# Optimization experiments

Hardware: AMD Instinct MI355X
Metric: run time of the kernel (lower is better)

## Reference

```python
import jax, jax.numpy as jnp
import numpy as np

B, C, L = 16, 128, 512
F = L // 2 + 1  # 257

def setup_inputs() -> dict:
    key = jax.random.key(0)
    k1, k2, k3 = jax.random.split(key, 3)
    x = jax.random.normal(k1, (B, C, L), dtype=jnp.float32)
    A = jax.random.normal(k2, (F, F), dtype=jnp.float32)
    gumbel_u = jax.random.uniform(k3, (B, C, C, 2), dtype=jnp.float32)
    return {"x": x, "A": A, "gumbel_u": gumbel_u}

def reference(x, A, gumbel_u):
    # --- calculate_prob_distance ---
    xf = jnp.abs(jnp.fft.rfft(x, axis=-1))                 # (b, c, f)
    diff = xf[:, None, :, :] - xf[:, :, None, :]           # (b, c, c, f): x1 - x2
    temp = jnp.einsum('bijf,gf->bijg', diff, A)            # diff @ A.T
    dist = jnp.sum(temp * temp, axis=-1)                   # (b, c, c)
    exp_dist = 1.0 / (dist + 3e-8)
    c = exp_dist.shape[-1]
    eye = jnp.eye(c, dtype=exp_dist.dtype)
    exp_dist = exp_dist * (1.0 - eye)
    exp_max = jax.lax.stop_gradient(jnp.max(exp_dist, axis=-1, keepdims=True))
    p = exp_dist / (exp_max + 1e-8)
    p = (p + eye) * 0.99
    # --- bernoulli_gumbel_rsample (hard gumbel-softmax, tau=1) ---
    logits = jnp.log(p + 1e-8) - jnp.log(1.0 - p + 1e-8)
    logits_pair = jnp.stack([logits, -logits], axis=-1)    # (b, c, c, 2)
    g = -jnp.log(-jnp.log(gumbel_u + 1e-20) + 1e-20)       # gumbel noise
    y = jax.nn.softmax(logits_pair + g, axis=-1)
    y_hard = jax.nn.one_hot(jnp.argmax(y, axis=-1), 2, dtype=y.dtype)
    samples = y_hard + y - jax.lax.stop_gradient(y)        # straight-through
    binary_mask = samples[..., 0]                          # (b, c, c)
    mask = binary_mask[:, None, :, :]                      # (b, 1, c, c)
    return mask
```

## Files before the change

### kernel.cpp

```cpp
#include <hip/hip_runtime.h>

#define LN   512
#define FB   257
#define CB   128
#define NROW 2048
#define KF   260
#define NP   272
#define GC   8

typedef double double4_t __attribute__((ext_vector_type(4)));

__global__ __launch_bounds__(256)
void k_prep(const float* __restrict__ A, double* __restrict__ At_d,
            double* __restrict__ xft, double2* __restrict__ tw) {
    const int bx = blockIdx.x;
    if (bx < 277) {
        int idx = bx * 256 + threadIdx.x;
        if (idx < KF * NP) {
            int f = idx / NP, g = idx - f * NP;
            At_d[idx] = (f < FB && g < FB) ? (double)A[g * FB + f] : 0.0;
        }
    } else if (bx < 301) {
        int idx = (bx - 277) * 256 + threadIdx.x;
        xft[(size_t)FB * NROW + idx] = 0.0;
    } else {
        int j = threadIdx.x;
        const double PI = 3.14159265358979323846264338327950288;
        double s, c;
        sincos(-2.0 * PI * (double)j / 512.0, &s, &c);
        tw[j] = make_double2(c, s);
    }
}

__global__ __launch_bounds__(128)
void k_fft2(const float* __restrict__ x,
            const double2* __restrict__ twg,
            double* __restrict__ xft) {
    __shared__ double2 a[LN];
    __shared__ double2 tw[256];
    const int pair = blockIdx.x;
    const int tid  = threadIdx.x;
    const int r0   = pair * 2;

    for (int t = tid; t < 256; t += 128) tw[t] = twg[t];

    const float* x0 = x + (size_t)r0 * LN;
    const float* x1 = x0 + LN;
    #pragma unroll
    for (int q = 0; q < 4; ++q) {
        int n = tid + 128 * q;
        int r = (int)(__brev((unsigned)n) >> 23);
        a[r] = make_double2((double)x0[n], (double)x1[n]);
    }
    __syncthreads();

    for (int s = 1; s <= 9; ++s) {
        const int half   = 1 << (s - 1);
        const int tshift = 9 - s;
        #pragma unroll
        for (int u = 0; u < 2; ++u) {
            int t   = tid + 128 * u;
            int k   = t & (half - 1);
            int grp = t >> (s - 1);
            int p0  = (grp << s) + k;
            int p1  = p0 + half;
            double2 w  = tw[k << tshift];
            double2 uu = a[p0];
            double2 v  = a[p1];
            double vr = v.x * w.x - v.y * w.y;
            double vi = v.x * w.y + v.y * w.x;
            a[p0] = make_double2(uu.x + vr, uu.y + vi);
            a[p1] = make_double2(uu.x - vr, uu.y - vi);
        }
        __syncthreads();
    }

    for (int k = tid; k < FB; k += 128) {
        int m = (LN - k) & (LN - 1);
        double2 zk = a[k];
        double2 zm = a[m];
        double xr = 0.5 * (zk.x + zm.x);
        double xi = 0.5 * (zk.y - zm.y);
        double yr = 0.5 * (zk.y + zm.y);
        double yi = 0.5 * (zm.x - zk.x);
        double m0 = sqrt(xr * xr + xi * xi);
        double m1 = sqrt(yr * yr + yi * yi);
        *(double2*)&xft[(size_t)k * NROW + r0] = make_double2(m0, m1);
    }
}

__global__ __launch_bounds__(256)
void k_zmat(const double* __restrict__ xft, const double* __restrict__ At_d,
            double* __restrict__ Zt) {
    const int bx  = blockIdx.x;
    const int tid = threadIdx.x;
    const int w   = tid >> 6;
    const int l   = tid & 63;
    const int q   = l >> 4;
    const int m   = l & 15;

    const int gt  = bx % 17;
    const int cht = (bx / 17) * 4 + w;
    const int g0  = gt * 16;
    const int ch0 = cht * 16;

    const double* pa = At_d + (size_t)q * NP + g0 + m;
    const double* pb = xft + (size_t)q * NROW + ch0 + m;

    double4_t acc = {0.0, 0.0, 0.0, 0.0};
    double a0 = pa[0],              b0 = pb[0];
    double a1 = pa[(size_t)4 * NP], b1 = pb[(size_t)4 * NROW];
    for (int it = 0; it < 63; ++it) {
        double a2 = pa[(size_t)(it + 2) * 4 * NP];
        double b2 = pb[(size_t)(it + 2) * 4 * NROW];
        acc = __builtin_amdgcn_mfma_f64_16x16x4f64(a0, b0, acc, 0, 0, 0);
        a0 = a1; a1 = a2; b0 = b1; b1 = b2;
    }
    acc = __builtin_amdgcn_mfma_f64_16x16x4f64(a0, b0, acc, 0, 0, 0);
    acc = __builtin_amdgcn_mfma_f64_16x16x4f64(a1, b1, acc, 0, 0, 0);

    const int b   = cht >> 3;
    const int chL = ((cht & 7) << 4) + m;
    double* zp = Zt + ((size_t)b * NP + g0 + 4 * q) * CB + chL;
    #pragma unroll
    for (int r = 0; r < 4; ++r) zp[(size_t)r * CB] = acc[r];
}

__global__ __launch_bounds__(256)
void k_dist(const double* __restrict__ Zt, double* __restrict__ dp,
            double* __restrict__ np_) {
    __shared__ double si[33][64];
    __shared__ double sj[33][64];
    const int bx = blockIdx.x;
    const int c  = bx & 7;
    const int jt = (bx >> 3) & 1;
    const int it = (bx >> 4) & 1;
    const int b  = bx >> 5;
    const int g0 = c * 32;
    const int gn = (c == 7) ? 33 : 32;
    const int i0 = it * 64, j0 = jt * 64;
    const int tid = threadIdx.x;
    const double* Zb = Zt + (size_t)b * NP * CB;

    for (int idx = tid; idx < gn * 64; idx += 256) {
        int gg = idx >> 6, ii = idx & 63;
        si[gg][ii] = Zb[(size_t)(g0 + gg) * CB + i0 + ii];
        sj[gg][ii] = Zb[(size_t)(g0 + gg) * CB + j0 + ii];
    }
    __syncthreads();

    if (it == 0 && tid < 64) {
        double na = 0.0;
        for (int gg = 0; gg < gn; ++gg) { double z = sj[gg][tid]; na += z * z; }
        np_[((size_t)b * GC + c) * CB + j0 + tid] = na;
    }

    const int tx = tid & 15, ty = tid >> 4;
    double acc[2][2][2][2];
    #pragma unroll
    for (int p = 0; p < 2; ++p)
        #pragma unroll
        for (int w = 0; w < 2; ++w)
            #pragma unroll
            for (int q = 0; q < 2; ++q)
                #pragma unroll
                for (int v = 0; v < 2; ++v) acc[p][w][q][v] = 0.0;

    #pragma unroll 4
    for (int gg = 0; gg < gn; ++gg) {
        double2 a0 = *(const double2*)&si[gg][2 * ty];
        double2 a1 = *(const double2*)&si[gg][32 + 2 * ty];
        double2 b0 = *(const double2*)&sj[gg][2 * tx];
        double2 b1 = *(const double2*)&sj[gg][32 + 2 * tx];
        acc[0][0][0][0] += a0.x * b0.x;
        acc[0][0][0][1] += a0.x * b0.y;
        acc[0][0][1][0] += a0.x * b1.x;
        acc[0][0][1][1] += a0.x * b1.y;
        acc[0][1][0][0] += a0.y * b0.x;
        acc[0][1][0][1] += a0.y * b0.y;
        acc[0][1][1][0] += a0.y * b1.x;
        acc[0][1][1][1] += a0.y * b1.y;
        acc[1][0][0][0] += a1.x * b0.x;
        acc[1][0][0][1] += a1.x * b0.y;
        acc[1][0][1][0] += a1.x * b1.x;
        acc[1][0][1][1] += a1.x * b1.y;
        acc[1][1][0][0] += a1.y * b0.x;
        acc[1][1][0][1] += a1.y * b0.y;
        acc[1][1][1][0] += a1.y * b1.x;
        acc[1][1][1][1] += a1.y * b1.y;
    }

    double* outp = dp + ((size_t)c * 16 + b) * CB * CB;
    #pragma unroll
    for (int p = 0; p < 2; ++p)
        #pragma unroll
        for (int w = 0; w < 2; ++w) {
            int row = i0 + p * 32 + 2 * ty + w;
            #pragma unroll
            for (int q = 0; q < 2; ++q)
                *(double2*)&outp[(size_t)row * CB + j0 + q * 32 + 2 * tx] =
                    make_double2(acc[p][w][q][0], acc[p][w][q][1]);
        }
}

__global__ __launch_bounds__(128)
void k_mask2(const double* __restrict__ dp, const double* __restrict__ np_,
             const float* __restrict__ gu, float* __restrict__ out) {
    __shared__ double sn[CB];
    __shared__ double wmax[2];
    const int bi = blockIdx.x;
    const int i  = bi & (CB - 1);
    const int b  = bi >> 7;
    const int j  = threadIdx.x;

    double G = 0.0, nj = 0.0;
    #pragma unroll
    for (int c = 0; c < GC; ++c) {
        G  += dp[(((size_t)c * 16 + b) * CB + i) * CB + j];
        nj += np_[((size_t)b * GC + c) * CB + j];
    }
    sn[j] = nj;
    __syncthreads();
    double ni = sn[i];
    double dist = ni + nj - 2.0 * G;

    double ed = 1.0 / (dist + 3e-8);
    if (j == i) ed = 0.0;

    double m = ed;
    #pragma unroll
    for (int off = 32; off >= 1; off >>= 1)
        m = fmax(m, __shfl_xor(m, off, 64));
    if ((j & 63) == 0) wmax[j >> 6] = m;
    __syncthreads();
    double emax = fmax(wmax[0], wmax[1]);

    double p = ed / (emax + 1e-8);
    if (j == i) p += 1.0;
    p *= 0.99;
    double L = log((p + 1e-8) / (1.0 - p + 1e-8));

    float2 u2 = ((const float2*)gu)[(size_t)bi * CB + j];
    double w0 = -log((double)u2.x + 1e-20);
    double w1 = -log((double)u2.y + 1e-20);
    double R = log((w0 + 1e-20) / (w1 + 1e-20));

    out[(size_t)bi * CB + j] = (2.0 * L >= R) ? 1.0f : 0.0f;
}

extern "C" void kernel_launch(void* const* d_in, const int* in_sizes, int n_in,
                              void* d_out, int out_size, void* d_ws, size_t ws_size,
                              hipStream_t stream) {
    const float* x  = (const float*)d_in[0];
    const float* A  = (const float*)d_in[1];
    const float* gu = (const float*)d_in[2];
    float* out = (float*)d_out;

    char* base = (char*)d_ws;
    const size_t szTw  = 4096;
    const size_t szAt  = (size_t)KF * NP * 8;
    const size_t szXft = (size_t)KF * NROW * 8;
    const size_t szZt  = (size_t)16 * NP * CB * 8;
    const size_t szDp  = (size_t)GC * 16 * CB * CB * 8;

    double2* tw   = (double2*)base;
    double* At_d  = (double*)(base + szTw);
    double* xft   = (double*)(base + szTw + szAt);
    double* Zt    = (double*)(base + szTw + szAt + szXft);
    double* dp    = (double*)(base + szTw + szAt + szXft + szZt);
    double* np    = (double*)(base + szTw + szAt + szXft + szZt + szDp);

    hipLaunchKernelGGL(k_prep,  dim3(302),      dim3(256), 0, stream, A, At_d, xft, tw);
    hipLaunchKernelGGL(k_fft2,  dim3(NROW / 2), dim3(128), 0, stream, x, tw, xft);
    hipLaunchKernelGGL(k_zmat,  dim3(544),      dim3(256), 0, stream, xft, At_d, Zt);
    hipLaunchKernelGGL(k_dist,  dim3(512),      dim3(256), 0, stream, Zt, dp, np);
    hipLaunchKernelGGL(k_mask2, dim3(NROW),     dim3(128), 0, stream, dp, np, gu, out);
}
```

Baseline: 50.80 us.

## Merge prep into FFT kernel and compute Gram matrix with f64 MFMA

```diff
diff --git a/kernel.cpp b/kernel.cpp
--- a/kernel.cpp
+++ b/kernel.cpp
@@ -6,43 +6,39 @@
 #define NROW 2048
 #define KF   260
 #define NP   272
-#define GC   8
 
 typedef double double4_t __attribute__((ext_vector_type(4)));
 
-__global__ __launch_bounds__(256)
-void k_prep(const float* __restrict__ A, double* __restrict__ At_d,
-            double* __restrict__ xft, double2* __restrict__ tw) {
-    const int bx = blockIdx.x;
-    if (bx < 277) {
-        int idx = bx * 256 + threadIdx.x;
-        if (idx < KF * NP) {
-            int f = idx / NP, g = idx - f * NP;
-            At_d[idx] = (f < FB && g < FB) ? (double)A[g * FB + f] : 0.0;
+__global__ __launch_bounds__(128)
+void k_fftprep(const float* __restrict__ x, const float* __restrict__ A,
+               double* __restrict__ xft, double* __restrict__ At_d) {
+    const int bx  = blockIdx.x;
+    const int tid = threadIdx.x;
+
+    if (bx >= 1024) {
+        if (bx < 1577) {
+            int idx = (bx - 1024) * 128 + tid;
+            if (idx < KF * NP) {
+                int f = idx / NP, g = idx - f * NP;
+                At_d[idx] = (f < FB && g < FB) ? (double)A[g * FB + f] : 0.0;
+            }
+        } else {
+            int idx = (bx - 1577) * 128 + tid;
+            xft[(size_t)FB * NROW + idx] = 0.0;
         }
-    } else if (bx < 301) {
-        int idx = (bx - 277) * 256 + threadIdx.x;
-        xft[(size_t)FB * NROW + idx] = 0.0;
-    } else {
-        int j = threadIdx.x;
-        const double PI = 3.14159265358979323846264338327950288;
-        double s, c;
-        sincos(-2.0 * PI * (double)j / 512.0, &s, &c);
-        tw[j] = make_double2(c, s);
-    }
-}
-
-__global__ __launch_bounds__(128)
-void k_fft2(const float* __restrict__ x,
-            const double2* __restrict__ twg,
-            double* __restrict__ xft) {
+        return;
+    }
+
     __shared__ double2 a[LN];
     __shared__ double2 tw[256];
-    const int pair = blockIdx.x;
-    const int tid  = threadIdx.x;
-    const int r0   = pair * 2;
-
-    for (int t = tid; t < 256; t += 128) tw[t] = twg[t];
+    const int r0 = bx * 2;
+
+    const double PI = 3.14159265358979323846264338327950288;
+    for (int t = tid; t < 256; t += 128) {
+        double s, c;
+        sincos(-2.0 * PI * (double)t / 512.0, &s, &c);
+        tw[t] = make_double2(c, s);
+    }
 
     const float* x0 = x + (size_t)r0 * LN;
     const float* x1 = x0 + LN;
@@ -121,90 +117,53 @@
 
     const int b   = cht >> 3;
     const int chL = ((cht & 7) << 4) + m;
-    double* zp = Zt + ((size_t)b * NP + g0 + 4 * q) * CB + chL;
-    #pragma unroll
-    for (int r = 0; r < 4; ++r) zp[(size_t)r * CB] = acc[r];
+    double* zp = Zt + ((size_t)b * NP + g0 + q) * CB + chL;
+    #pragma unroll
+    for (int r = 0; r < 4; ++r) zp[(size_t)(4 * r) * CB] = acc[r];
 }
 
 __global__ __launch_bounds__(256)
-void k_dist(const double* __restrict__ Zt, double* __restrict__ dp,
-            double* __restrict__ np_) {
-    __shared__ double si[33][64];
-    __shared__ double sj[33][64];
-    const int bx = blockIdx.x;
-    const int c  = bx & 7;
-    const int jt = (bx >> 3) & 1;
-    const int it = (bx >> 4) & 1;
-    const int b  = bx >> 5;
-    const int g0 = c * 32;
-    const int gn = (c == 7) ? 33 : 32;
-    const int i0 = it * 64, j0 = jt * 64;
+void k_gram(const double* __restrict__ Zt, double* __restrict__ G) {
+    const int bx  = blockIdx.x;
     const int tid = threadIdx.x;
-    const double* Zb = Zt + (size_t)b * NP * CB;
-
-    for (int idx = tid; idx < gn * 64; idx += 256) {
-        int gg = idx >> 6, ii = idx & 63;
-        si[gg][ii] = Zb[(size_t)(g0 + gg) * CB + i0 + ii];
-        sj[gg][ii] = Zb[(size_t)(g0 + gg) * CB + j0 + ii];
-    }
-    __syncthreads();
-
-    if (it == 0 && tid < 64) {
-        double na = 0.0;
-        for (int gg = 0; gg < gn; ++gg) { double z = sj[gg][tid]; na += z * z; }
-        np_[((size_t)b * GC + c) * CB + j0 + tid] = na;
-    }
-
-    const int tx = tid & 15, ty = tid >> 4;
-    double acc[2][2][2][2];
-    #pragma unroll
-    for (int p = 0; p < 2; ++p)
-        #pragma unroll
-        for (int w = 0; w < 2; ++w)
-            #pragma unroll
-            for (int q = 0; q < 2; ++q)
-                #pragma unroll
-                for (int v = 0; v < 2; ++v) acc[p][w][q][v] = 0.0;
-
-    #pragma unroll 4
-    for (int gg = 0; gg < gn; ++gg) {
-        double2 a0 = *(const double2*)&si[gg][2 * ty];
-        double2 a1 = *(const double2*)&si[gg][32 + 2 * ty];
-        double2 b0 = *(const double2*)&sj[gg][2 * tx];
-        double2 b1 = *(const double2*)&sj[gg][32 + 2 * tx];
-        acc[0][0][0][0] += a0.x * b0.x;
-        acc[0][0][0][1] += a0.x * b0.y;
-        acc[0][0][1][0] += a0.x * b1.x;
-        acc[0][0][1][1] += a0.x * b1.y;
-        acc[0][1][0][0] += a0.y * b0.x;
-        acc[0][1][0][1] += a0.y * b0.y;
-        acc[0][1][1][0] += a0.y * b1.x;
-        acc[0][1][1][1] += a0.y * b1.y;
-        acc[1][0][0][0] += a1.x * b0.x;
-        acc[1][0][0][1] += a1.x * b0.y;
-        acc[1][0][1][0] += a1.x * b1.x;
-        acc[1][0][1][1] += a1.x * b1.y;
-        acc[1][1][0][0] += a1.y * b0.x;
-        acc[1][1][0][1] += a1.y * b0.y;
-        acc[1][1][1][0] += a1.y * b1.x;
-        acc[1][1][1][1] += a1.y * b1.y;
-    }
-
-    double* outp = dp + ((size_t)c * 16 + b) * CB * CB;
-    #pragma unroll
-    for (int p = 0; p < 2; ++p)
-        #pragma unroll
-        for (int w = 0; w < 2; ++w) {
-            int row = i0 + p * 32 + 2 * ty + w;
-            #pragma unroll
-            for (int q = 0; q < 2; ++q)
-                *(double2*)&outp[(size_t)row * CB + j0 + q * 32 + 2 * tx] =
-                    make_double2(acc[p][w][q][0], acc[p][w][q][1]);
-        }
+    const int w   = tid >> 6;
+    const int l   = tid & 63;
+    const int q   = l >> 4;
+    const int m   = l & 15;
+
+    const int b  = bx >> 4;
+    const int it = (bx >> 1) & 7;
+    const int jt = (bx & 1) * 4 + w;
+    const int i0 = it * 16, j0 = jt * 16;
+
+    const double* zb = Zt + (size_t)b * NP * CB;
+    const double* pa = zb + (size_t)q * CB + i0 + m;
+    const double* pb = zb + (size_t)q * CB + j0 + m;
+
+    double4_t acc = {0.0, 0.0, 0.0, 0.0};
+    double a0 = pa[0],    b0 = pb[0];
+    double a1 = pa[512],  b1 = pb[512];
+    double a2 = pa[1024], b2 = pb[1024];
+    double a3 = pa[1536], b3 = pb[1536];
+    for (int t2 = 0; t2 < 61; ++t2) {
+        double an = pa[(size_t)(t2 + 4) * 512];
+        double bn = pb[(size_t)(t2 + 4) * 512];
+        acc = __builtin_amdgcn_mfma_f64_16x16x4f64(a0, b0, acc, 0, 0, 0);
+        a0 = a1; a1 = a2; a2 = a3; a3 = an;
+        b0 = b1; b1 = b2; b2 = b3; b3 = bn;
+    }
+    acc = __builtin_amdgcn_mfma_f64_16x16x4f64(a0, b0, acc, 0, 0, 0);
+    acc = __builtin_amdgcn_mfma_f64_16x16x4f64(a1, b1, acc, 0, 0, 0);
+    acc = __builtin_amdgcn_mfma_f64_16x16x4f64(a2, b2, acc, 0, 0, 0);
+    acc = __builtin_amdgcn_mfma_f64_16x16x4f64(a3, b3, acc, 0, 0, 0);
+
+    double* gp = G + ((size_t)(b * CB + i0 + q)) * CB + j0 + m;
+    #pragma unroll
+    for (int r = 0; r < 4; ++r) gp[(size_t)(4 * r) * CB] = acc[r];
 }
 
 __global__ __launch_bounds__(128)
-void k_mask2(const double* __restrict__ dp, const double* __restrict__ np_,
+void k_mask2(const double* __restrict__ G,
              const float* __restrict__ gu, float* __restrict__ out) {
     __shared__ double sn[CB];
     __shared__ double wmax[2];
@@ -213,16 +172,12 @@
     const int b  = bi >> 7;
     const int j  = threadIdx.x;
 
-    double G = 0.0, nj = 0.0;
-    #pragma unroll
-    for (int c = 0; c < GC; ++c) {
-        G  += dp[(((size_t)c * 16 + b) * CB + i) * CB + j];
-        nj += np_[((size_t)b * GC + c) * CB + j];
-    }
+    double nj = G[((size_t)(b * CB + j)) * CB + j];
+    double Gv = G[(size_t)bi * CB + j];
     sn[j] = nj;
     __syncthreads();
     double ni = sn[i];
-    double dist = ni + nj - 2.0 * G;
+    double dist = ni + nj - 2.0 * Gv;
 
     double ed = 1.0 / (dist + 3e-8);
     if (j == i) ed = 0.0;
@@ -257,22 +212,17 @@
     float* out = (float*)d_out;
 
     char* base = (char*)d_ws;
-    const size_t szTw  = 4096;
     const size_t szAt  = (size_t)KF * NP * 8;
     const size_t szXft = (size_t)KF * NROW * 8;
     const size_t szZt  = (size_t)16 * NP * CB * 8;
-    const size_t szDp  = (size_t)GC * 16 * CB * CB * 8;
-
-    double2* tw   = (double2*)base;
-    double* At_d  = (double*)(base + szTw);
-    double* xft   = (double*)(base + szTw + szAt);
-    double* Zt    = (double*)(base + szTw + szAt + szXft);
-    double* dp    = (double*)(base + szTw + szAt + szXft + szZt);
-    double* np    = (double*)(base + szTw + szAt + szXft + szZt + szDp);
-
-    hipLaunchKernelGGL(k_prep,  dim3(302),      dim3(256), 0, stream, A, At_d, xft, tw);
-    hipLaunchKernelGGL(k_fft2,  dim3(NROW / 2), dim3(128), 0, stream, x, tw, xft);
-    hipLaunchKernelGGL(k_zmat,  dim3(544),      dim3(256), 0, stream, xft, At_d, Zt);
-    hipLaunchKernelGGL(k_dist,  dim3(512),      dim3(256), 0, stream, Zt, dp, np);
-    hipLaunchKernelGGL(k_mask2, dim3(NROW),     dim3(128), 0, stream, dp, np, gu, out);
-}
+
+    double* At_d = (double*)base;
+    double* xft  = (double*)(base + szAt);
+    double* Zt   = (double*)(base + szAt + szXft);
+    double* G    = (double*)(base + szAt + szXft + szZt);
+
+    hipLaunchKernelGGL(k_fftprep, dim3(1625), dim3(128), 0, stream, x, A, xft, At_d);
+    hipLaunchKernelGGL(k_zmat,    dim3(544),  dim3(256), 0, stream, xft, At_d, Zt);
+    hipLaunchKernelGGL(k_gram,    dim3(256),  dim3(256), 0, stream, Zt, G);
+    hipLaunchKernelGGL(k_mask2,   dim3(2048), dim3(128), 0, stream, G, gu, out);
+}
```

New measurement: 53.68 us. 5.7% more time.
